# Kernel tuning notes

Measured on AMD Instinct MI355X. Metric: run time of the kernel, lower is better.

The kernel has to match this reference:

```python
import jax, jax.numpy as jnp
import numpy as np

N = 100_000   # total vertices
E = 1_600_000 # total directed edges
B = 64        # graphs in batch
HID = 128
DM = 256
EPS = 1e-5


def _linear_init(k, fan_in, fan_out):
    lim = 1.0 / np.sqrt(fan_in)
    kw, kb = jax.random.split(k)
    W = jax.random.uniform(kw, (fan_in, fan_out), minval=-lim, maxval=lim, dtype=jnp.float32)
    b = jax.random.uniform(kb, (fan_out,), minval=-lim, maxval=lim, dtype=jnp.float32)
    return W, b


def setup_inputs() -> dict:
    key = jax.random.key(0)
    ks = jax.random.split(key, 8)
    W_in, b_in = _linear_init(ks[0], 3, HID)
    W1, b1 = _linear_init(ks[1], HID, HID)
    W2, b2 = _linear_init(ks[2], HID, HID)
    W3, b3 = _linear_init(ks[3], HID, HID)
    W_out, b_out = _linear_init(ks[4], HID, DM)
    vertices = jax.random.normal(ks[5], (N, 3), dtype=jnp.float32)
    edge_index = jax.random.randint(ks[6], (2, E), 0, N)
    batch = jnp.sort(jax.random.randint(ks[7], (N,), 0, B))
    gamma = jnp.ones((DM,), jnp.float32)
    beta = jnp.zeros((DM,), jnp.float32)
    return dict(vertices=vertices, edge_index=edge_index, batch=batch,
                W_in=W_in, b_in=b_in, W1=W1, b1=b1, W2=W2, b2=b2, W3=W3, b3=b3,
                W_out=W_out, b_out=b_out, gamma=gamma, beta=beta)


def _gcn_conv(x, W, b, src, dst):
    # PyG GCNConv: add self-loops, sym-normalize by deg^{-1/2}, aggregate at dst.
    h = x @ W  # [N, HID]
    deg = jnp.zeros((x.shape[0],), x.dtype).at[dst].add(1.0) + 1.0  # +1 self-loop
    dinv = jax.lax.rsqrt(deg)
    msg = h[src] * (dinv[src] * dinv[dst])[:, None]       # [E, HID] gather+scale
    agg = jnp.zeros_like(h).at[dst].add(msg)               # scatter-add
    agg = agg + h * (dinv * dinv)[:, None]                 # self-loop contribution
    return agg + b


def reference(vertices, edge_index, batch, W_in, b_in, W1, b1, W2, b2, W3, b3, W_out, b_out, gamma, beta):
    src, dst = edge_index[0], edge_index[1]
    x = vertices @ W_in + b_in
    for W, b in ((W1, b1), (W2, b2), (W3, b3)):
        x = jax.nn.relu(_gcn_conv(x, W, b, src, dst))
    # global_mean_pool over batch segments
    summ = jax.ops.segment_sum(x, batch, num_segments=B)
    cnt = jax.ops.segment_sum(jnp.ones((x.shape[0], 1), x.dtype), batch, num_segments=B)
    pooled = summ / jnp.maximum(cnt, 1.0)
    y = pooled @ W_out + b_out
    mu = jnp.mean(y, axis=-1, keepdims=True)
    var = jnp.var(y, axis=-1, keepdims=True)
    return (y - mu) * jax.lax.rsqrt(var + EPS) * gamma + beta
```

## Files before the change

### kernel.cpp

```cpp
#include <hip/hip_runtime.h>

constexpr int NV = 100000;
constexpr int NE = 1600000;
constexpr int NB = 64;
constexpr int HD = 128;
constexpr int DM = 256;
#define EPSLN 1e-5f

constexpr int DPB   = 512;
constexpr int NBUCK = (NV + DPB - 1) / DPB;
constexpr int BCAP  = 16384;
constexpr int EPB   = 4096;
constexpr int NEB   = (NE + EPB - 1) / EPB;

typedef short bf16x8 __attribute__((ext_vector_type(8)));
typedef float f32x4 __attribute__((ext_vector_type(4)));

__device__ inline unsigned short f2b(float f) {
    union { float f; unsigned u; } x; x.f = f;
    unsigned r = x.u + 0x7FFF + ((x.u >> 16) & 1);
    return (unsigned short)(r >> 16);
}
__device__ inline float b2f(unsigned short h) {
    union { unsigned u; float f; } x; x.u = (unsigned)h << 16;
    return x.f;
}

__global__ __launch_bounds__(256) void k_bscatter(const int* __restrict__ ei,
                                                  int* __restrict__ bcursor,
                                                  int* __restrict__ ebuf) {
    __shared__ int h[NBUCK];
    __shared__ int lbase[NBUCK];
    int t = threadIdx.x;
    for (int i = t; i < NBUCK; i += 256) h[i] = 0;
    __syncthreads();
    int base = blockIdx.x * EPB;
    int s[16], d[16], rk[16];
    #pragma unroll
    for (int j = 0; j < 16; ++j) {
        int idx = base + j * 256 + t;
        if (idx < NE) {
            s[j] = ei[idx];
            d[j] = ei[NE + idx];
            rk[j] = atomicAdd(&h[d[j] >> 9], 1);
        } else d[j] = -1;
    }
    __syncthreads();
    for (int i = t; i < NBUCK; i += 256) {
        int c = h[i];
        if (c) lbase[i] = atomicAdd(&bcursor[i], c);
    }
    __syncthreads();
    #pragma unroll
    for (int j = 0; j < 16; ++j)
        if (d[j] >= 0) {
            int b = d[j] >> 9;
            ebuf[(b << 14) + lbase[b] + rk[j]] = (s[j] << 9) | (d[j] & 511);
        }
}

__global__ __launch_bounds__(256) void k_bcsr(const int* __restrict__ ebuf,
                                              const int* __restrict__ bcursor,
                                              int* __restrict__ degi,
                                              float* __restrict__ dinv,
                                              int* __restrict__ rowstart,
                                              int* __restrict__ csr) {
    __shared__ int h[DPB];
    __shared__ int sdata[256];
    int b = blockIdx.x, t = threadIdx.x, d0 = b * DPB;
    for (int i = t; i < DPB; i += 256) h[i] = 0;
    __syncthreads();
    int e0 = b << 14;
    int e1 = e0 + bcursor[b];
    for (int e = e0 + t; e < e1; e += 256) atomicAdd(&h[ebuf[e] & 511], 1);
    __syncthreads();
    int a = h[2 * t], c = h[2 * t + 1];
    sdata[t] = a + c;
    __syncthreads();
    for (int off = 1; off < 256; off <<= 1) {
        int v = sdata[t];
        int add = (t >= off) ? sdata[t - off] : 0;
        __syncthreads();
        sdata[t] = v + add;
        __syncthreads();
    }
    int excl = (t == 0) ? 0 : sdata[t - 1];
    int base = e0;
    int v0 = d0 + 2 * t, v1 = v0 + 1;
    if (v0 < NV) { rowstart[v0] = base + excl;     degi[v0] = a; dinv[v0] = rsqrtf((float)a + 1.0f); }
    if (v1 < NV) { rowstart[v1] = base + excl + a; degi[v1] = c; dinv[v1] = rsqrtf((float)c + 1.0f); }
    h[2 * t]     = base + excl;
    h[2 * t + 1] = base + excl + a;
    __syncthreads();
    for (int e = e0 + t; e < e1; e += 256) {
        int p = ebuf[e];
        int slot = atomicAdd(&h[p & 511], 1);
        csr[slot] = p >> 9;
    }
}

__global__ __launch_bounds__(256) void k_prep(const float* __restrict__ verts,
                                              const float* __restrict__ Win,
                                              const float* __restrict__ bin,
                                              const float* __restrict__ W1,
                                              const float* __restrict__ W2,
                                              const float* __restrict__ W3,
                                              unsigned short* __restrict__ Hb,
                                              unsigned short* __restrict__ Wt) {
    int t = threadIdx.x;
    if (blockIdx.x >= 1024) {
        int idx = (blockIdx.x - 1024) * 256 + t;
        if (idx < 2 * HD * HD) {
            int l = idx >> 14, r = idx & 16383;
            const float* W = (l == 0) ? W2 : W3;
            int n = r >> 7, k = r & 127;
            Wt[(l << 14) + n * HD + k] = f2b(W[k * HD + n]);
        }
        return;
    }
    __shared__ float Wc[3 * HD];
    __shared__ float bc[HD];
    if (t < HD) {
        float w0 = 0.f, w1 = 0.f, w2 = 0.f, bv = 0.f;
        for (int k = 0; k < HD; ++k) {
            float w = W1[k * HD + t];
            w0 = fmaf(Win[k], w, w0);
            w1 = fmaf(Win[128 + k], w, w1);
            w2 = fmaf(Win[256 + k], w, w2);
            bv = fmaf(bin[k], w, bv);
        }
        Wc[t] = w0; Wc[128 + t] = w1; Wc[256 + t] = w2; bc[t] = bv;
    }
    __syncthreads();
    for (int idx = blockIdx.x * 256 + t; idx < NV * HD; idx += 1024 * 256) {
        int v = idx >> 7, c = idx & 127;
        float a = verts[v * 3 + 0], b = verts[v * 3 + 1], d = verts[v * 3 + 2];
        Hb[idx] = f2b(bc[c] + a * Wc[c] + b * Wc[128 + c] + d * Wc[256 + c]);
    }
}

__global__ __launch_bounds__(256) void k_gemm_mfma(const unsigned short* __restrict__ Xb,
                                                   const unsigned short* __restrict__ Wt,
                                                   unsigned short* __restrict__ Hb) {
    __shared__ __align__(16) unsigned short Ws[128 * 132];
    __shared__ __align__(16) unsigned short hs[4][16][136];
    int t = threadIdx.x;
    {
        int row = t >> 1;
        int half = (t & 1) << 6;
        const unsigned short* src = Wt + row * HD + half;
        unsigned short* dst = &Ws[row * 132 + half];
        #pragma unroll
        for (int i = 0; i < 8; ++i)
            *(bf16x8*)(dst + i * 8) = *(const bf16x8*)(src + i * 8);
    }
    int wave = t >> 6;
    int lane = t & 63;
    int r = lane & 15;
    int g = lane >> 4;
    int row0 = blockIdx.x * 64 + wave * 16;
    int arow = row0 + r;
    bool valid = arow < NV;

    bf16x8 afrag[4];
    const unsigned short* xp = Xb + (size_t)arow * HD + g * 8;
    #pragma unroll
    for (int ks = 0; ks < 4; ++ks) {
        if (valid) afrag[ks] = *(const bf16x8*)(xp + ks * 32);
        else       afrag[ks] = bf16x8{0, 0, 0, 0, 0, 0, 0, 0};
    }
    __syncthreads();

    #pragma unroll
    for (int nt = 0; nt < 8; ++nt) {
        f32x4 acc = {0.f, 0.f, 0.f, 0.f};
        #pragma unroll
        for (int ks = 0; ks < 4; ++ks) {
            bf16x8 bfrag = *(const bf16x8*)&Ws[(nt * 16 + r) * 132 + g * 8 + ks * 32];
            acc = __builtin_amdgcn_mfma_f32_16x16x32_bf16(afrag[ks], bfrag, acc, 0, 0, 0);
        }
        #pragma unroll
        for (int j = 0; j < 4; ++j)
            hs[wave][g * 4 + j][nt * 16 + r] = f2b(acc[j]);
    }
    int row = lane >> 2;
    int grow = row0 + row;
    #pragma unroll
    for (int k = 0; k < 4; ++k) {
        int c = (lane & 3) + k * 4;
        bf16x8 val = *(const bf16x8*)&hs[wave][row][c * 8];
        if (grow < NV)
            *(bf16x8*)(Hb + (size_t)grow * HD + c * 8) = val;
    }
}

__global__ __launch_bounds__(256) void k_agg(const unsigned short* __restrict__ H,
                                             const float* __restrict__ dinv,
                                             const int* __restrict__ rowstart,
                                             const int* __restrict__ degi,
                                             const int* __restrict__ csr_src,
                                             const float* __restrict__ bias,
                                             unsigned short* __restrict__ Xo) {
    int gtid = blockIdx.x * 256 + threadIdx.x;
    int v = gtid >> 6;
    if (v >= NV) return;
    int lane = threadIdx.x & 63;
    int q = lane >> 4;
    int l4 = lane & 15;
    float di = dinv[v];
    int rs = rowstart[v], len = degi[v];
    float a[8];
    if (q == 0) {
        float sc = di * di;
        bf16x8 hv = *(const bf16x8*)(H + (size_t)v * HD + l4 * 8);
        #pragma unroll
        for (int jj = 0; jj < 8; ++jj) a[jj] = b2f((unsigned short)hv[jj]) * sc;
    } else {
        #pragma unroll
        for (int jj = 0; jj < 8; ++jj) a[jj] = 0.f;
    }
    int cnt = (len - q + 3) >> 2;
    int idx = rs + q;
    int j = 0;
    for (; j + 1 < cnt; j += 2) {
        int s0 = csr_src[idx], s1 = csr_src[idx + 4];
        idx += 8;
        float w0 = dinv[s0] * di, w1 = dinv[s1] * di;
        bf16x8 h0 = *(const bf16x8*)(H + (size_t)s0 * HD + l4 * 8);
        bf16x8 h1 = *(const bf16x8*)(H + (size_t)s1 * HD + l4 * 8);
        #pragma unroll
        for (int jj = 0; jj < 8; ++jj) {
            a[jj] = fmaf(b2f((unsigned short)h0[jj]), w0, a[jj]);
            a[jj] = fmaf(b2f((unsigned short)h1[jj]), w1, a[jj]);
        }
    }
    if (j < cnt) {
        int s0 = csr_src[idx];
        float w0 = dinv[s0] * di;
        bf16x8 h0 = *(const bf16x8*)(H + (size_t)s0 * HD + l4 * 8);
        #pragma unroll
        for (int jj = 0; jj < 8; ++jj)
            a[jj] = fmaf(b2f((unsigned short)h0[jj]), w0, a[jj]);
    }
    #pragma unroll
    for (int jj = 0; jj < 8; ++jj) {
        a[jj] += __shfl_xor(a[jj], 16);
        a[jj] += __shfl_xor(a[jj], 32);
    }
    if (q == 0) {
        bf16x8 ov;
        #pragma unroll
        for (int jj = 0; jj < 8; ++jj)
            ov[jj] = (short)f2b(fmaxf(a[jj] + bias[l4 * 8 + jj], 0.f));
        *(bf16x8*)(Xo + (size_t)v * HD + l4 * 8) = ov;
    }
}

__global__ __launch_bounds__(256) void k_pool(const unsigned short* __restrict__ X,
                                              const int* __restrict__ batch,
                                              float* __restrict__ pool,
                                              int* __restrict__ cnt) {
    constexpr int CHUNK = (NV + 2047) / 2048;
    __shared__ float lp[2][HD];
    __shared__ int binfo[2];
    int t = threadIdx.x;
    int v0 = blockIdx.x * CHUNK;
    if (v0 >= NV) return;
    int vend = min(v0 + CHUNK, NV);
    if (t < 2 * HD) ((float*)lp)[t] = 0.f;
    if (t == 0) { binfo[0] = batch[v0]; binfo[1] = batch[vend - 1]; }
    __syncthreads();
    int b0 = binfo[0], b1 = binfo[1];
    int cg = t & 15;
    int ro = t >> 4;
    if (b1 - b0 <= 1) {
        float a0[8] = {}, a1[8] = {};
        for (int v = v0 + ro; v < vend; v += 16) {
            bf16x8 x = *(const bf16x8*)(X + (size_t)v * HD + cg * 8);
            if (batch[v] == b0) {
                #pragma unroll
                for (int jj = 0; jj < 8; ++jj) a0[jj] += b2f((unsigned short)x[jj]);
            } else {
                #pragma unroll
                for (int jj = 0; jj < 8; ++jj) a1[jj] += b2f((unsigned short)x[jj]);
            }
        }
        #pragma unroll
        for (int jj = 0; jj < 8; ++jj) {
            atomicAdd(&lp[0][cg * 8 + jj], a0[jj]);
            if (b1 != b0) atomicAdd(&lp[1][cg * 8 + jj], a1[jj]);
        }
        __syncthreads();
        int slot = t >> 7, col = t & 127;
        if (slot == 0 || b1 != b0)
            atomicAdd(&pool[(slot ? b1 : b0) * HD + col], lp[slot][col]);
    } else {
        float a[8] = {};
        int cur = -1;
        for (int v = v0 + ro; v < vend; v += 16) {
            int bb = batch[v];
            if (bb != cur) {
                if (cur >= 0) {
                    #pragma unroll
                    for (int jj = 0; jj < 8; ++jj) {
                        atomicAdd(&pool[cur * HD + cg * 8 + jj], a[jj]);
                        a[jj] = 0.f;
                    }
                }
                cur = bb;
            }
            bf16x8 x = *(const bf16x8*)(X + (size_t)v * HD + cg * 8);
            #pragma unroll
            for (int jj = 0; jj < 8; ++jj) a[jj] += b2f((unsigned short)x[jj]);
        }
        if (cur >= 0) {
            #pragma unroll
            for (int jj = 0; jj < 8; ++jj)
                atomicAdd(&pool[cur * HD + cg * 8 + jj], a[jj]);
        }
    }
    if (t == 0) {
        int prev = batch[v0], c0 = 0;
        for (int v = v0; v < vend; ++v) {
            int bb = batch[v];
            if (bb != prev) { atomicAdd(&cnt[prev], c0); prev = bb; c0 = 0; }
            ++c0;
        }
        atomicAdd(&cnt[prev], c0);
    }
}

__global__ __launch_bounds__(256) void k_out(const float* __restrict__ pool,
                                             const int* __restrict__ cnt,
                                             const float* __restrict__ Wout,
                                             const float* __restrict__ bout,
                                             const float* __restrict__ gamma,
                                             const float* __restrict__ beta,
                                             float* __restrict__ out) {
    __shared__ float ps[HD];
    __shared__ float red[DM];
    int g = blockIdx.x, t = threadIdx.x;
    if (t < HD) {
        float cn = fmaxf((float)cnt[g], 1.0f);
        ps[t] = pool[g * HD + t] / cn;
    }
    __syncthreads();
    float acc = bout[t];
    #pragma unroll 8
    for (int k = 0; k < HD; ++k) acc = fmaf(ps[k], Wout[k * DM + t], acc);
    red[t] = acc; __syncthreads();
    for (int s2 = 128; s2 > 0; s2 >>= 1) {
        if (t < s2) red[t] += red[t + s2];
        __syncthreads();
    }
    float mu = red[0] * (1.0f / DM);
    __syncthreads();
    float d = acc - mu;
    red[t] = d * d; __syncthreads();
    for (int s2 = 128; s2 > 0; s2 >>= 1) {
        if (t < s2) red[t] += red[t + s2];
        __syncthreads();
    }
    float var = red[0] * (1.0f / DM);
    out[g * DM + t] = d * rsqrtf(var + EPSLN) * gamma[t] + beta[t];
}

extern "C" void kernel_launch(void* const* d_in, const int* in_sizes, int n_in,
                              void* d_out, int out_size, void* d_ws, size_t ws_size,
                              hipStream_t stream) {
    const float* verts = (const float*)d_in[0];
    const int*   ei    = (const int*)d_in[1];
    const int*   batch = (const int*)d_in[2];
    const float* Win   = (const float*)d_in[3];
    const float* bin   = (const float*)d_in[4];
    const float* W1    = (const float*)d_in[5];
    const float* b1    = (const float*)d_in[6];
    const float* W2    = (const float*)d_in[7];
    const float* b2    = (const float*)d_in[8];
    const float* W3    = (const float*)d_in[9];
    const float* b3    = (const float*)d_in[10];
    const float* Wout  = (const float*)d_in[11];
    const float* bout  = (const float*)d_in[12];
    const float* gamma = (const float*)d_in[13];
    const float* beta  = (const float*)d_in[14];
    float* out = (float*)d_out;

    char* wp = (char*)d_ws;
    auto alloc = [&](size_t bytes) -> char* {
        char* p = wp;
        wp += (bytes + 255) & ~(size_t)255;
        return p;
    };
    unsigned short* bufA = (unsigned short*)alloc((size_t)NV * HD * 2);
    unsigned short* bufB = (unsigned short*)alloc((size_t)NV * HD * 2);
    unsigned short* Wt   = (unsigned short*)alloc((size_t)2 * HD * HD * 2);
    int*   degi     = (int*)alloc((size_t)NV * 4);
    float* dinv     = (float*)alloc((size_t)NV * 4);
    int*   rowstart = (int*)alloc((size_t)NV * 4);
    int*   csr      = (int*)alloc((size_t)NBUCK * BCAP * 4);
    int*   ebuf     = (int*)alloc((size_t)NBUCK * BCAP * 4);
    char*  zblock   = alloc(1024 + (size_t)NB * HD * 4 + 1024);
    int*   bcursor  = (int*)zblock;
    float* pool     = (float*)(zblock + 1024);
    int*   cnt      = (int*)(zblock + 1024 + (size_t)NB * HD * 4);

    hipMemsetAsync(zblock, 0, 1024 + (size_t)NB * HD * 4 + 1024, stream);

    k_bscatter<<<NEB, 256, 0, stream>>>(ei, bcursor, ebuf);
    k_bcsr<<<NBUCK, 256, 0, stream>>>(ebuf, bcursor, degi, dinv, rowstart, csr);

    k_prep<<<1152, 256, 0, stream>>>(verts, Win, bin, W1, W2, W3, bufA, Wt);

    int aggrid = (int)(((size_t)NV * 64 + 255) / 256);
    k_agg<<<aggrid, 256, 0, stream>>>(bufA, dinv, rowstart, degi, csr, b1, bufB);
    k_gemm_mfma<<<(NV + 63) / 64, 256, 0, stream>>>(bufB, Wt, bufA);
    k_agg<<<aggrid, 256, 0, stream>>>(bufA, dinv, rowstart, degi, csr, b2, bufB);
    k_gemm_mfma<<<(NV + 63) / 64, 256, 0, stream>>>(bufB, Wt + (size_t)HD * HD, bufA);
    k_agg<<<aggrid, 256, 0, stream>>>(bufA, dinv, rowstart, degi, csr, b3, bufB);

    k_pool<<<2048, 256, 0, stream>>>(bufB, batch, pool, cnt);
    k_out<<<NB, 256, 0, stream>>>(pool, cnt, Wout, bout, gamma, beta, out);
}
```

Baseline: 345.5 us.

## Fuse edge bucketing with input prep and cache bucket edges in LDS for CSR

```diff
diff --git a/kernel.cpp b/kernel.cpp
--- a/kernel.cpp
+++ b/kernel.cpp
@@ -10,8 +10,11 @@
 constexpr int DPB   = 512;
 constexpr int NBUCK = (NV + DPB - 1) / DPB;
 constexpr int BCAP  = 16384;
-constexpr int EPB   = 4096;
-constexpr int NEB   = (NE + EPB - 1) / EPB;
+constexpr int EPB2  = 2048;
+constexpr int NEB2  = (NE + EPB2 - 1) / EPB2;
+constexpr int H1B   = 1024;
+constexpr int WTB   = 128;
+constexpr int LCAP  = 12288;
 
 typedef short bf16x8 __attribute__((ext_vector_type(8)));
 typedef float f32x4 __attribute__((ext_vector_type(4)));
@@ -26,58 +29,104 @@
     return x.f;
 }
 
-__global__ __launch_bounds__(256) void k_bscatter(const int* __restrict__ ei,
-                                                  int* __restrict__ bcursor,
-                                                  int* __restrict__ ebuf) {
-    __shared__ int h[NBUCK];
-    __shared__ int lbase[NBUCK];
+__global__ __launch_bounds__(256) void k_init(const float* __restrict__ verts,
+                                              const float* __restrict__ Win,
+                                              const float* __restrict__ bin,
+                                              const float* __restrict__ W1,
+                                              const float* __restrict__ W2,
+                                              const float* __restrict__ W3,
+                                              const int* __restrict__ ei,
+                                              int* __restrict__ bcursor,
+                                              int* __restrict__ ebuf,
+                                              unsigned short* __restrict__ Hb,
+                                              unsigned short* __restrict__ Wt) {
     int t = threadIdx.x;
-    for (int i = t; i < NBUCK; i += 256) h[i] = 0;
-    __syncthreads();
-    int base = blockIdx.x * EPB;
-    int s[16], d[16], rk[16];
-    #pragma unroll
-    for (int j = 0; j < 16; ++j) {
-        int idx = base + j * 256 + t;
-        if (idx < NE) {
-            s[j] = ei[idx];
-            d[j] = ei[NE + idx];
-            rk[j] = atomicAdd(&h[d[j] >> 9], 1);
-        } else d[j] = -1;
-    }
-    __syncthreads();
-    for (int i = t; i < NBUCK; i += 256) {
-        int c = h[i];
-        if (c) lbase[i] = atomicAdd(&bcursor[i], c);
-    }
-    __syncthreads();
-    #pragma unroll
-    for (int j = 0; j < 16; ++j)
-        if (d[j] >= 0) {
-            int b = d[j] >> 9;
-            ebuf[(b << 14) + lbase[b] + rk[j]] = (s[j] << 9) | (d[j] & 511);
-        }
-}
-
-__global__ __launch_bounds__(256) void k_bcsr(const int* __restrict__ ebuf,
+    int bid = blockIdx.x;
+    if (bid < NEB2) {
+        __shared__ int h[NBUCK];
+        __shared__ int lbase[NBUCK];
+        for (int i = t; i < NBUCK; i += 256) h[i] = 0;
+        __syncthreads();
+        int base = bid * EPB2;
+        int s[8], d[8], rk[8];
+        #pragma unroll
+        for (int j = 0; j < 8; ++j) {
+            int idx = base + j * 256 + t;
+            if (idx < NE) {
+                s[j] = ei[idx];
+                d[j] = ei[NE + idx];
+                rk[j] = atomicAdd(&h[d[j] >> 9], 1);
+            } else d[j] = -1;
+        }
+        __syncthreads();
+        for (int i = t; i < NBUCK; i += 256) {
+            int c = h[i];
+            if (c) lbase[i] = atomicAdd(&bcursor[i], c);
+        }
+        __syncthreads();
+        #pragma unroll
+        for (int j = 0; j < 8; ++j)
+            if (d[j] >= 0) {
+                int b = d[j] >> 9;
+                ebuf[(b << 14) + lbase[b] + rk[j]] = (s[j] << 9) | (d[j] & 511);
+            }
+        return;
+    }
+    if (bid < NEB2 + H1B) {
+        __shared__ float Wc[3 * HD];
+        __shared__ float bc[HD];
+        if (t < HD) {
+            float w0 = 0.f, w1 = 0.f, w2 = 0.f, bv = 0.f;
+            for (int k = 0; k < HD; ++k) {
+                float w = W1[k * HD + t];
+                w0 = fmaf(Win[k], w, w0);
+                w1 = fmaf(Win[128 + k], w, w1);
+                w2 = fmaf(Win[256 + k], w, w2);
+                bv = fmaf(bin[k], w, bv);
+            }
+            Wc[t] = w0; Wc[128 + t] = w1; Wc[256 + t] = w2; bc[t] = bv;
+        }
+        __syncthreads();
+        for (int idx = (bid - NEB2) * 256 + t; idx < NV * HD; idx += H1B * 256) {
+            int v = idx >> 7, c = idx & 127;
+            float a = verts[v * 3 + 0], b = verts[v * 3 + 1], d = verts[v * 3 + 2];
+            Hb[idx] = f2b(bc[c] + a * Wc[c] + b * Wc[128 + c] + d * Wc[256 + c]);
+        }
+        return;
+    }
+    int idx = (bid - NEB2 - H1B) * 256 + t;
+    if (idx < 2 * HD * HD) {
+        int l = idx >> 14, r = idx & 16383;
+        const float* W = (l == 0) ? W2 : W3;
+        int n = r >> 7, k = r & 127;
+        Wt[(l << 14) + n * HD + k] = f2b(W[k * HD + n]);
+    }
+}
+
+__global__ __launch_bounds__(512) void k_bcsr(const int* __restrict__ ebuf,
                                               const int* __restrict__ bcursor,
                                               int* __restrict__ degi,
                                               float* __restrict__ dinv,
                                               int* __restrict__ rowstart,
                                               int* __restrict__ csr) {
+    __shared__ int els[LCAP];
     __shared__ int h[DPB];
-    __shared__ int sdata[256];
+    __shared__ int sdata[DPB];
     int b = blockIdx.x, t = threadIdx.x, d0 = b * DPB;
-    for (int i = t; i < DPB; i += 256) h[i] = 0;
+    if (t < DPB) h[t] = 0;
     __syncthreads();
     int e0 = b << 14;
-    int e1 = e0 + bcursor[b];
-    for (int e = e0 + t; e < e1; e += 256) atomicAdd(&h[ebuf[e] & 511], 1);
-    __syncthreads();
-    int a = h[2 * t], c = h[2 * t + 1];
-    sdata[t] = a + c;
-    __syncthreads();
-    for (int off = 1; off < 256; off <<= 1) {
+    int n = bcursor[b];
+    for (int i = t; i < n; i += 512) {
+        int p = ebuf[e0 + i];
+        if (i < LCAP) els[i] = p;
+        atomicAdd(&h[p & 511], 1);
+    }
+    __syncthreads();
+    int a = h[t];
+    sdata[t] = a;
+    __syncthreads();
+    for (int off = 1; off < 512; off <<= 1) {
         int v = sdata[t];
         int add = (t >= off) ? sdata[t - off] : 0;
         __syncthreads();
@@ -85,57 +134,18 @@
         __syncthreads();
     }
     int excl = (t == 0) ? 0 : sdata[t - 1];
-    int base = e0;
-    int v0 = d0 + 2 * t, v1 = v0 + 1;
-    if (v0 < NV) { rowstart[v0] = base + excl;     degi[v0] = a; dinv[v0] = rsqrtf((float)a + 1.0f); }
-    if (v1 < NV) { rowstart[v1] = base + excl + a; degi[v1] = c; dinv[v1] = rsqrtf((float)c + 1.0f); }
-    h[2 * t]     = base + excl;
-    h[2 * t + 1] = base + excl + a;
-    __syncthreads();
-    for (int e = e0 + t; e < e1; e += 256) {
-        int p = ebuf[e];
+    int v0 = d0 + t;
+    if (v0 < NV) {
+        rowstart[v0] = e0 + excl;
+        degi[v0] = a;
+        dinv[v0] = rsqrtf((float)a + 1.0f);
+    }
+    h[t] = e0 + excl;
+    __syncthreads();
+    for (int i = t; i < n; i += 512) {
+        int p = (i < LCAP) ? els[i] : ebuf[e0 + i];
         int slot = atomicAdd(&h[p & 511], 1);
         csr[slot] = p >> 9;
-    }
-}
-
-__global__ __launch_bounds__(256) void k_prep(const float* __restrict__ verts,
-                                              const float* __restrict__ Win,
-                                              const float* __restrict__ bin,
-                                              const float* __restrict__ W1,
-                                              const float* __restrict__ W2,
-                                              const float* __restrict__ W3,
-                                              unsigned short* __restrict__ Hb,
-                                              unsigned short* __restrict__ Wt) {
-    int t = threadIdx.x;
-    if (blockIdx.x >= 1024) {
-        int idx = (blockIdx.x - 1024) * 256 + t;
-        if (idx < 2 * HD * HD) {
-            int l = idx >> 14, r = idx & 16383;
-            const float* W = (l == 0) ? W2 : W3;
-            int n = r >> 7, k = r & 127;
-            Wt[(l << 14) + n * HD + k] = f2b(W[k * HD + n]);
-        }
-        return;
-    }
-    __shared__ float Wc[3 * HD];
-    __shared__ float bc[HD];
-    if (t < HD) {
-        float w0 = 0.f, w1 = 0.f, w2 = 0.f, bv = 0.f;
-        for (int k = 0; k < HD; ++k) {
-            float w = W1[k * HD + t];
-            w0 = fmaf(Win[k], w, w0);
-            w1 = fmaf(Win[128 + k], w, w1);
-            w2 = fmaf(Win[256 + k], w, w2);
-            bv = fmaf(bin[k], w, bv);
-        }
-        Wc[t] = w0; Wc[128 + t] = w1; Wc[256 + t] = w2; bc[t] = bv;
-    }
-    __syncthreads();
-    for (int idx = blockIdx.x * 256 + t; idx < NV * HD; idx += 1024 * 256) {
-        int v = idx >> 7, c = idx & 127;
-        float a = verts[v * 3 + 0], b = verts[v * 3 + 1], d = verts[v * 3 + 2];
-        Hb[idx] = f2b(bc[c] + a * Wc[c] + b * Wc[128 + c] + d * Wc[256 + c]);
     }
 }
 
@@ -406,10 +416,9 @@
 
     hipMemsetAsync(zblock, 0, 1024 + (size_t)NB * HD * 4 + 1024, stream);
 
-    k_bscatter<<<NEB, 256, 0, stream>>>(ei, bcursor, ebuf);
-    k_bcsr<<<NBUCK, 256, 0, stream>>>(ebuf, bcursor, degi, dinv, rowstart, csr);
-
-    k_prep<<<1152, 256, 0, stream>>>(verts, Win, bin, W1, W2, W3, bufA, Wt);
+    k_init<<<NEB2 + H1B + WTB, 256, 0, stream>>>(verts, Win, bin, W1, W2, W3,
+                                                 ei, bcursor, ebuf, bufA, Wt);
+    k_bcsr<<<NBUCK, 512, 0, stream>>>(ebuf, bcursor, degi, dinv, rowstart, csr);
 
     int aggrid = (int)(((size_t)NV * 64 + 255) / 256);
     k_agg<<<aggrid, 256, 0, stream>>>(bufA, dinv, rowstart, degi, csr, b1, bufB);
```

Result: no change. 339.5 us (-1.7%).
